# Kernel tuning notes

Measured on AMD Instinct MI355X. Metric: run time of the kernel, lower is better.

## Reference

```python
import jax, jax.numpy as jnp
import numpy as np

MIN_NORM = 1e-15
BALL_EPS = 4e-3  # torch float32 ball epsilon in KGEmb
E, R, D = 500000, 1000, 256
NQ = 200000
INIT = 1e-3
SCALE = float(1.0 / np.sqrt(D))


def setup_inputs() -> dict:
    key = jax.random.key(0)
    ks = jax.random.split(key, 7)
    heads = jax.random.randint(ks[0], (NQ, 1), 0, E)
    rels = jax.random.randint(ks[1], (NQ, 1), 0, R)
    tails = jax.random.randint(ks[2], (NQ, 1), 0, E)
    queries = jnp.concatenate([heads, rels, tails], axis=1)
    return {
        "queries": queries,
        "entity_emb": INIT * jax.random.normal(ks[3], (E, D), jnp.float32),
        "rel_emb": INIT * jax.random.normal(ks[4], (R, 2 * D), jnp.float32),
        "bias_head": jnp.zeros((E, 1), jnp.float32),
        "bias_tail": jnp.zeros((E, 1), jnp.float32),
        "c": jnp.ones((R, 1), jnp.float32),
        "att_rel_emb": 2.0 * jax.random.uniform(ks[5], (R, 2 * D), jnp.float32) - 1.0,
        "context_emb": INIT * jax.random.normal(ks[6], (R, D), jnp.float32),
    }


def artanh(x):
    x = jnp.clip(x, -1.0 + 1e-5, 1.0 - 1e-5)
    return 0.5 * (jnp.log1p(x) - jnp.log1p(-x))


def givens_rotations(r, x):
    # r, x: [n, d]; operate on d/2 independent 2-vectors
    n, d = x.shape
    g = r.reshape(n, d // 2, 2)
    g = g / jnp.maximum(jnp.linalg.norm(g, axis=-1, keepdims=True), MIN_NORM)
    xr = x.reshape(n, d // 2, 2)
    rot = jnp.stack(
        [g[..., 0] * xr[..., 0] - g[..., 1] * xr[..., 1],
         g[..., 0] * xr[..., 1] + g[..., 1] * xr[..., 0]], axis=-1)
    return rot.reshape(n, d)


def givens_reflection(r, x):
    n, d = x.shape
    g = r.reshape(n, d // 2, 2)
    g = g / jnp.maximum(jnp.linalg.norm(g, axis=-1, keepdims=True), MIN_NORM)
    xr = x.reshape(n, d // 2, 2)
    ref = jnp.stack(
        [g[..., 0] * xr[..., 0] + g[..., 1] * xr[..., 1],
         g[..., 1] * xr[..., 0] - g[..., 0] * xr[..., 1]], axis=-1)
    return ref.reshape(n, d)


def project(x, c):
    norm = jnp.maximum(jnp.linalg.norm(x, axis=-1, keepdims=True), MIN_NORM)
    maxnorm = (1.0 - BALL_EPS) / jnp.sqrt(c)
    return jnp.where(norm > maxnorm, x / norm * maxnorm, x)


def expmap0(u, c):
    sqrt_c = jnp.sqrt(c)
    u_norm = jnp.maximum(jnp.linalg.norm(u, axis=-1, keepdims=True), MIN_NORM)
    gamma_1 = jnp.tanh(sqrt_c * u_norm) * u / (sqrt_c * u_norm)
    return project(gamma_1, c)


def mobius_add(x, y, c):
    x2 = jnp.sum(x * x, axis=-1, keepdims=True)
    y2 = jnp.sum(y * y, axis=-1, keepdims=True)
    xy = jnp.sum(x * y, axis=-1, keepdims=True)
    num = (1.0 + 2.0 * c * xy + c * y2) * x + (1.0 - c * x2) * y
    denom = 1.0 + 2.0 * c * xy + (c ** 2) * x2 * y2
    return num / jnp.maximum(denom, MIN_NORM)


def hyp_distance(x, v, c):
    # x: point on ball, v: Euclidean (tangent) embedding; train mode (paired rows)
    sqrt_c = jnp.sqrt(c)
    vnorm = jnp.maximum(jnp.linalg.norm(v, axis=-1, keepdims=True), MIN_NORM)
    xv = jnp.sum(x * v / vnorm, axis=-1, keepdims=True)
    gamma = jnp.tanh(sqrt_c * vnorm) / vnorm
    x2 = jnp.sum(x * x, axis=-1, keepdims=True)
    c1 = 1.0 - 2.0 * c * gamma * xv + c * gamma ** 2
    c2 = 1.0 - c * x2
    num = jnp.sqrt(jnp.maximum((c1 ** 2) * x2 + (c2 ** 2) * (gamma ** 2)
                               - 2.0 * c1 * c2 * gamma * xv, 0.0))
    denom = jnp.maximum(1.0 - 2.0 * c * gamma * xv + (c ** 2) * (gamma ** 2) * x2, MIN_NORM)
    return 2.0 * artanh(sqrt_c * num / denom) / sqrt_c


def atth_forward(queries, entity_emb, rel_emb, bias_head, bias_tail, c,
                 att_rel_emb, context_emb):
    h, r, t = queries[:, 0], queries[:, 1], queries[:, 2]
    c_q = jax.nn.softplus(c[r])                       # [n, 1]
    head = entity_emb[h]                              # [n, D]
    rot_mat, ref_mat = jnp.split(att_rel_emb[r], 2, axis=1)
    rot_q = givens_rotations(rot_mat, head)           # [n, D]
    ref_q = givens_reflection(ref_mat, head)          # [n, D]
    cands = jnp.stack([ref_q, rot_q], axis=1)         # [n, 2, D]
    ctx = context_emb[r][:, None, :]                  # [n, 1, D]
    att_w = jax.nn.softmax(
        jnp.sum(ctx * cands * SCALE, axis=-1, keepdims=True), axis=1)  # [n, 2, 1]
    att_q = jnp.sum(att_w * cands, axis=1)            # [n, D]
    lhs = expmap0(att_q, c_q)
    rel = jnp.split(rel_emb[r], 2, axis=1)[0]
    rel = expmap0(rel, c_q)
    res = project(mobius_add(lhs, rel, c_q), c_q)
    dist2 = hyp_distance(res, entity_emb[t], c_q) ** 2
    predictions = bias_head[h] + bias_tail[t] + dist2  # [n, 1]
    factors = (head, rel_emb[r], entity_emb[t])
    return (predictions,) + factors


def reference(queries, entity_emb, rel_emb, bias_head, bias_tail, c,
              att_rel_emb, context_emb):
    return atth_forward(queries, entity_emb, rel_emb, bias_head, bias_tail, c,
                        att_rel_emb, context_emb)
```

## Files before the change

### kernel.cpp

```cpp
#include <hip/hip_runtime.h>
#include <math.h>

#define MIN_NORM 1e-15f
#define BALL_EPS 0.004f

constexpr int D  = 256;
constexpr int R  = 1000;
constexpr int NQ = 200000;
constexpr float SCALE = 0.0625f;

typedef float  f32x4  __attribute__((ext_vector_type(4)));
typedef unsigned short u16x8 __attribute__((ext_vector_type(8)));

__device__ __forceinline__ void nt_store4(float* p, f32x4 v) {
    __builtin_nontemporal_store(v, (f32x4*)p);
}
__device__ __forceinline__ f32x4 ld4(const float* p) { return *(const f32x4*)p; }

__device__ __forceinline__ unsigned short f2bf(float x) {
    unsigned int u = __float_as_uint(x);
    u += 0x7fffu + ((u >> 16) & 1u);
    return (unsigned short)(u >> 16);
}
__device__ __forceinline__ float bf2f(unsigned short u) {
    return __uint_as_float(((unsigned int)u) << 16);
}

__device__ __forceinline__ void half_sum4(float& a, float& b, float& c, float& d) {
    #pragma unroll
    for (int off = 16; off > 0; off >>= 1) {
        a += __shfl_xor(a, off, 64);
        b += __shfl_xor(b, off, 64);
        c += __shfl_xor(c, off, 64);
        d += __shfl_xor(d, off, 64);
    }
}
__device__ __forceinline__ void half_sum3(float& a, float& b, float& c) {
    #pragma unroll
    for (int off = 16; off > 0; off >>= 1) {
        a += __shfl_xor(a, off, 64);
        b += __shfl_xor(b, off, 64);
        c += __shfl_xor(c, off, 64);
    }
}

__device__ __forceinline__ void unpack8(f32x4 a, f32x4 b, float* d) {
    d[0] = a.x; d[1] = a.y; d[2] = a.z; d[3] = a.w;
    d[4] = b.x; d[5] = b.y; d[6] = b.z; d[7] = b.w;
}

__device__ __forceinline__ float tanh_pos(float x) {
    const float e = __expf(-2.0f * x);
    return (1.0f - e) / (1.0f + e);
}

__global__ __launch_bounds__(64) void prep_kernel(
    const float* __restrict__ rel_emb,
    const float* __restrict__ c_arr,
    const float* __restrict__ att_rel_emb,
    const float* __restrict__ context_emb,
    float* __restrict__ ws_scal,
    unsigned short* __restrict__ ws_rot,
    unsigned short* __restrict__ ws_ref,
    unsigned short* __restrict__ ws_ctx)
{
    const int r    = blockIdx.x;
    const int lane = threadIdx.x;

    const float craw   = c_arr[r];
    const float cq     = fmaxf(craw, 0.0f) + log1pf(__expf(-fabsf(craw)));
    const float sqrt_c = sqrtf(cq);
    const float maxnorm = (1.0f - BALL_EPS) / sqrt_c;

    const float* am = att_rel_emb + (size_t)r * 2 * D + lane * 4;
    const float* cb = context_emb + (size_t)r * D     + lane * 4;
    const float* rr = rel_emb     + (size_t)r * 2 * D + lane * 4;

    float rotn[4], refn[4];
    #pragma unroll
    for (int p = 0; p < 2; ++p) {
        const float a0 = am[2*p], a1 = am[2*p+1];
        float inv = rsqrtf(fmaxf(a0*a0 + a1*a1, 1e-30f));
        rotn[2*p] = a0*inv; rotn[2*p+1] = a1*inv;
        const float b0 = am[D + 2*p], b1 = am[D + 2*p+1];
        inv = rsqrtf(fmaxf(b0*b0 + b1*b1, 1e-30f));
        refn[2*p] = b0*inv; refn[2*p+1] = b1*inv;
    }

    float url2 = 0.0f;
    float ctxs[4];
    #pragma unroll
    for (int j = 0; j < 4; ++j) {
        ctxs[j] = cb[j] * SCALE;
        const float v = rr[j];
        url2 += v * v;
    }
    #pragma unroll
    for (int off = 32; off > 0; off >>= 1) url2 += __shfl_xor(url2, off, 64);

    const float url  = fmaxf(sqrtf(url2), MIN_NORM);
    const float facB = tanh_pos(sqrt_c * url) / (sqrt_c * url);
    const float nB   = facB * url;
    const float sB   = facB * ((nB > maxnorm) ? maxnorm / nB : 1.0f);
    const float y2   = sB * sB * url2;

    #pragma unroll
    for (int j = 0; j < 4; ++j) {
        ws_rot[(size_t)r * D + lane*4 + j] = f2bf(rotn[j]);
        ws_ref[(size_t)r * D + lane*4 + j] = f2bf(refn[j]);
        ws_ctx[(size_t)r * D + lane*4 + j] = f2bf(ctxs[j]);
    }
    if (lane == 0) {
        float* s = ws_scal + (size_t)r * 8;
        s[0] = cq; s[1] = sqrt_c; s[2] = maxnorm; s[3] = sB; s[4] = y2;
    }
}

__global__ __launch_bounds__(256) void atth_kernel(
    const int*   __restrict__ queries,
    const float* __restrict__ entity_emb,
    const float* __restrict__ rel_emb,
    const float* __restrict__ bias_head,
    const float* __restrict__ bias_tail,
    const float* __restrict__ ws_scal,
    const unsigned short* __restrict__ ws_rot,
    const unsigned short* __restrict__ ws_ref,
    const unsigned short* __restrict__ ws_ctx,
    float*       __restrict__ out)
{
    const int lane = threadIdx.x & 63;
    const int hl   = lane & 31;
    const int qid  = blockIdx.x * 8 + (threadIdx.x >> 5);
    if (qid >= NQ) return;

    const int h = queries[qid * 3 + 0];
    const int r = queries[qid * 3 + 1];
    const int t = queries[qid * 3 + 2];

    const float* sc = ws_scal + (size_t)r * 8;
    const float cq = sc[0], sqrt_c = sc[1], maxnorm = sc[2], sB = sc[3], y2 = sc[4];

    const int e8 = hl * 8;

    const float* eh = entity_emb + (size_t)h * D     + e8;
    const float* et = entity_emb + (size_t)t * D     + e8;
    const float* rr = rel_emb    + (size_t)r * 2 * D + e8;

    const f32x4 h0 = ld4(eh);     const f32x4 h1 = ld4(eh + 4);
    const f32x4 t0 = ld4(et);     const f32x4 t1 = ld4(et + 4);
    const f32x4 r0 = ld4(rr);     const f32x4 r1 = ld4(rr + 4);
    const f32x4 r2 = ld4(rr + D); const f32x4 r3 = ld4(rr + D + 4);
    const u16x8 rotv = *(const u16x8*)(ws_rot + (size_t)r * D + e8);
    const u16x8 refv = *(const u16x8*)(ws_ref + (size_t)r * D + e8);
    const u16x8 ctxv = *(const u16x8*)(ws_ctx + (size_t)r * D + e8);

    float* out_pred = out;
    float* out_head = out + (size_t)NQ;
    float* out_rel  = out + (size_t)NQ + (size_t)NQ * D;
    float* out_tail = out + (size_t)NQ + (size_t)NQ * D + (size_t)NQ * 2 * D;

    nt_store4(out_head + (size_t)qid * D         + e8,     h0);
    nt_store4(out_head + (size_t)qid * D         + e8 + 4, h1);
    nt_store4(out_rel  + (size_t)qid * 2 * D     + e8,     r0);
    nt_store4(out_rel  + (size_t)qid * 2 * D     + e8 + 4, r1);
    nt_store4(out_rel  + (size_t)qid * 2 * D + D + e8,     r2);
    nt_store4(out_rel  + (size_t)qid * 2 * D + D + e8 + 4, r3);
    nt_store4(out_tail + (size_t)qid * D         + e8,     t0);
    nt_store4(out_tail + (size_t)qid * D         + e8 + 4, t1);

    float hd[8], tl[8], rl[8];
    unpack8(h0, h1, hd);
    unpack8(t0, t1, tl);
    unpack8(r0, r1, rl);

    float rq[8], fq[8];
    #pragma unroll
    for (int p = 0; p < 4; ++p) {
        const int i0 = 2*p, i1 = 2*p + 1;
        const float g0 = bf2f(rotv[i0]), g1 = bf2f(rotv[i1]);
        rq[i0] = g0 * hd[i0] - g1 * hd[i1];
        rq[i1] = g0 * hd[i1] + g1 * hd[i0];
        const float e0 = bf2f(refv[i0]), e1 = bf2f(refv[i1]);
        fq[i0] = e0 * hd[i0] + e1 * hd[i1];
        fq[i1] = e1 * hd[i0] - e0 * hd[i1];
    }

    float sref = 0.0f, srot = 0.0f, sv = 0.0f, rtl = 0.0f;
    #pragma unroll
    for (int j = 0; j < 8; ++j) {
        const float cxj = bf2f(ctxv[j]);
        sref += cxj * fq[j];
        srot += cxj * rq[j];
        sv   += tl[j] * tl[j];
        rtl  += rl[j] * tl[j];
    }
    half_sum4(sref, srot, sv, rtl);

    const float mx   = fmaxf(sref, srot);
    const float eref = __expf(sref - mx), erot = __expf(srot - mx);
    const float inv_se = 1.0f / (eref + erot);
    const float wref = eref * inv_se, wrot = erot * inv_se;

    float att[8];
    #pragma unroll
    for (int j = 0; j < 8; ++j) att[j] = wref * fq[j] + wrot * rq[j];

    float u2 = 0.0f, adr = 0.0f, atl = 0.0f;
    #pragma unroll
    for (int j = 0; j < 8; ++j) {
        u2  += att[j] * att[j];
        adr += att[j] * rl[j];
        atl += att[j] * tl[j];
    }
    half_sum3(u2, adr, atl);

    const float u    = fmaxf(sqrtf(u2), MIN_NORM);
    const float facA = tanh_pos(sqrt_c * u) / (sqrt_c * u);
    const float nA   = facA * u;
    const float sA   = facA * ((nA > maxnorm) ? maxnorm / nA : 1.0f);
    const float x2   = sA * sA * u2;

    const float xy = sA * sB * adr;

    const float ka  = 1.0f + 2.0f * cq * xy + cq * y2;
    const float kb  = 1.0f - cq * x2;
    const float den = fmaxf(1.0f + 2.0f * cq * xy + cq * cq * x2 * y2, MIN_NORM);
    const float pA  = ka * sA / den;
    const float pB  = kb * sB / den;

    const float url2_from_y2 = 0.0f;
    (void)url2_from_y2;
    const float rl2 = y2 / fmaxf(sB * sB, 1e-30f);
    const float rn2 = pA*pA*u2 + 2.0f*pA*pB*adr + pB*pB*rl2;
    const float nrm = fmaxf(sqrtf(rn2), MIN_NORM);
    const float pr  = (nrm > maxnorm) ? maxnorm / nrm : 1.0f;
    const float rx2 = rn2 * pr * pr;

    const float vnorm = fmaxf(sqrtf(sv), MIN_NORM);
    const float sxv   = (pA * atl + pB * rtl) * pr;
    const float xv    = sxv / vnorm;
    const float gamma = tanh_pos(sqrt_c * vnorm) / vnorm;
    const float k1 = 1.0f - 2.0f * cq * gamma * xv + cq * gamma * gamma;
    const float k2 = 1.0f - cq * rx2;
    const float num = sqrtf(fmaxf(k1*k1*rx2 + k2*k2*gamma*gamma
                                  - 2.0f*k1*k2*gamma*xv, 0.0f));
    const float dden = fmaxf(1.0f - 2.0f*cq*gamma*xv + cq*cq*gamma*gamma*rx2, MIN_NORM);
    float arg = sqrt_c * num / dden;
    arg = fminf(fmaxf(arg, -1.0f + 1e-5f), 1.0f - 1e-5f);
    const float ath  = 0.5f * __logf((1.0f + arg) / (1.0f - arg));
    const float dist = 2.0f * ath / sqrt_c;
    const float dist2 = dist * dist;

    if (hl == 0) {
        __builtin_nontemporal_store(bias_head[h] + bias_tail[t] + dist2, out_pred + qid);
    }
}

extern "C" void kernel_launch(void* const* d_in, const int* in_sizes, int n_in,
                              void* d_out, int out_size, void* d_ws, size_t ws_size,
                              hipStream_t stream) {
    const int*   queries     = (const int*)  d_in[0];
    const float* entity_emb  = (const float*)d_in[1];
    const float* rel_emb     = (const float*)d_in[2];
    const float* bias_head   = (const float*)d_in[3];
    const float* bias_tail   = (const float*)d_in[4];
    const float* c_arr       = (const float*)d_in[5];
    const float* att_rel_emb = (const float*)d_in[6];
    const float* context_emb = (const float*)d_in[7];
    float* out = (float*)d_out;

    float*          ws_scal = (float*)d_ws;
    unsigned short* ws_rot  = (unsigned short*)(ws_scal + (size_t)R * 8);
    unsigned short* ws_ref  = ws_rot + (size_t)R * D;
    unsigned short* ws_ctx  = ws_ref + (size_t)R * D;

    prep_kernel<<<R, 64, 0, stream>>>(rel_emb, c_arr, att_rel_emb, context_emb,
                                      ws_scal, ws_rot, ws_ref, ws_ctx);

    const int queries_per_block = 8;
    const int grid = (NQ + queries_per_block - 1) / queries_per_block;
    atth_kernel<<<grid, 256, 0, stream>>>(queries, entity_emb, rel_emb,
                                          bias_head, bias_tail,
                                          ws_scal, ws_rot, ws_ref, ws_ctx, out);
}
```

Measured before the change: 304.8 us.

## Split rel_emb gather-copy into its own kernel and use bf16 rel in compute

Moves the copy of rel_emb rows into the output into a separate kernel where each wave copies one full 2D-float row. The main kernel instead reads a bf16 copy of the first half of the relation embedding prepared per relation, and a precomputed squared norm. This is meant to make the output write simpler and shrink the main kernel's per-query reads and stores. The cost is one extra kernel launch that re-reads the queries, and reduced precision for the relation vector in the distance math.

```diff
diff --git a/kernel.cpp b/kernel.cpp
--- a/kernel.cpp
+++ b/kernel.cpp
@@ -62,7 +62,8 @@
     float* __restrict__ ws_scal,
     unsigned short* __restrict__ ws_rot,
     unsigned short* __restrict__ ws_ref,
-    unsigned short* __restrict__ ws_ctx)
+    unsigned short* __restrict__ ws_ctx,
+    unsigned short* __restrict__ ws_rl)
 {
     const int r    = blockIdx.x;
     const int lane = threadIdx.x;
@@ -88,12 +89,12 @@
     }
 
     float url2 = 0.0f;
-    float ctxs[4];
+    float rlv[4], ctxs[4];
     #pragma unroll
     for (int j = 0; j < 4; ++j) {
         ctxs[j] = cb[j] * SCALE;
-        const float v = rr[j];
-        url2 += v * v;
+        rlv[j]  = rr[j];
+        url2 += rlv[j] * rlv[j];
     }
     #pragma unroll
     for (int off = 32; off > 0; off >>= 1) url2 += __shfl_xor(url2, off, 64);
@@ -109,23 +110,43 @@
         ws_rot[(size_t)r * D + lane*4 + j] = f2bf(rotn[j]);
         ws_ref[(size_t)r * D + lane*4 + j] = f2bf(refn[j]);
         ws_ctx[(size_t)r * D + lane*4 + j] = f2bf(ctxs[j]);
+        ws_rl [(size_t)r * D + lane*4 + j] = f2bf(rlv[j]);
     }
     if (lane == 0) {
         float* s = ws_scal + (size_t)r * 8;
         s[0] = cq; s[1] = sqrt_c; s[2] = maxnorm; s[3] = sB; s[4] = y2;
-    }
+        s[5] = url2;
+    }
+}
+
+__global__ __launch_bounds__(256) void copy_rel_kernel(
+    const int*   __restrict__ queries,
+    const float* __restrict__ rel_emb,
+    float*       __restrict__ out_rel)
+{
+    const int wave = threadIdx.x >> 6;
+    const int lane = threadIdx.x & 63;
+    const int q = blockIdx.x * 4 + wave;
+    if (q >= NQ) return;
+    const int r = queries[q * 3 + 1];
+    const float* src = rel_emb + (size_t)r * 2 * D + lane * 8;
+    float*       dst = out_rel + (size_t)q * 2 * D + lane * 8;
+    const f32x4 a = ld4(src);
+    const f32x4 b = ld4(src + 4);
+    nt_store4(dst,     a);
+    nt_store4(dst + 4, b);
 }
 
 __global__ __launch_bounds__(256) void atth_kernel(
     const int*   __restrict__ queries,
     const float* __restrict__ entity_emb,
-    const float* __restrict__ rel_emb,
     const float* __restrict__ bias_head,
     const float* __restrict__ bias_tail,
     const float* __restrict__ ws_scal,
     const unsigned short* __restrict__ ws_rot,
     const unsigned short* __restrict__ ws_ref,
     const unsigned short* __restrict__ ws_ctx,
+    const unsigned short* __restrict__ ws_rl,
     float*       __restrict__ out)
 {
     const int lane = threadIdx.x & 63;
@@ -139,39 +160,34 @@
 
     const float* sc = ws_scal + (size_t)r * 8;
     const float cq = sc[0], sqrt_c = sc[1], maxnorm = sc[2], sB = sc[3], y2 = sc[4];
+    const float rl2 = sc[5];
 
     const int e8 = hl * 8;
 
-    const float* eh = entity_emb + (size_t)h * D     + e8;
-    const float* et = entity_emb + (size_t)t * D     + e8;
-    const float* rr = rel_emb    + (size_t)r * 2 * D + e8;
+    const float* eh = entity_emb + (size_t)h * D + e8;
+    const float* et = entity_emb + (size_t)t * D + e8;
 
     const f32x4 h0 = ld4(eh);     const f32x4 h1 = ld4(eh + 4);
     const f32x4 t0 = ld4(et);     const f32x4 t1 = ld4(et + 4);
-    const f32x4 r0 = ld4(rr);     const f32x4 r1 = ld4(rr + 4);
-    const f32x4 r2 = ld4(rr + D); const f32x4 r3 = ld4(rr + D + 4);
     const u16x8 rotv = *(const u16x8*)(ws_rot + (size_t)r * D + e8);
     const u16x8 refv = *(const u16x8*)(ws_ref + (size_t)r * D + e8);
     const u16x8 ctxv = *(const u16x8*)(ws_ctx + (size_t)r * D + e8);
+    const u16x8 rlv  = *(const u16x8*)(ws_rl  + (size_t)r * D + e8);
 
     float* out_pred = out;
     float* out_head = out + (size_t)NQ;
-    float* out_rel  = out + (size_t)NQ + (size_t)NQ * D;
     float* out_tail = out + (size_t)NQ + (size_t)NQ * D + (size_t)NQ * 2 * D;
 
-    nt_store4(out_head + (size_t)qid * D         + e8,     h0);
-    nt_store4(out_head + (size_t)qid * D         + e8 + 4, h1);
-    nt_store4(out_rel  + (size_t)qid * 2 * D     + e8,     r0);
-    nt_store4(out_rel  + (size_t)qid * 2 * D     + e8 + 4, r1);
-    nt_store4(out_rel  + (size_t)qid * 2 * D + D + e8,     r2);
-    nt_store4(out_rel  + (size_t)qid * 2 * D + D + e8 + 4, r3);
-    nt_store4(out_tail + (size_t)qid * D         + e8,     t0);
-    nt_store4(out_tail + (size_t)qid * D         + e8 + 4, t1);
+    nt_store4(out_head + (size_t)qid * D + e8,     h0);
+    nt_store4(out_head + (size_t)qid * D + e8 + 4, h1);
+    nt_store4(out_tail + (size_t)qid * D + e8,     t0);
+    nt_store4(out_tail + (size_t)qid * D + e8 + 4, t1);
 
     float hd[8], tl[8], rl[8];
     unpack8(h0, h1, hd);
     unpack8(t0, t1, tl);
-    unpack8(r0, r1, rl);
+    #pragma unroll
+    for (int j = 0; j < 8; ++j) rl[j] = bf2f(rlv[j]);
 
     float rq[8], fq[8];
     #pragma unroll
@@ -228,9 +244,6 @@
     const float pA  = ka * sA / den;
     const float pB  = kb * sB / den;
 
-    const float url2_from_y2 = 0.0f;
-    (void)url2_from_y2;
-    const float rl2 = y2 / fmaxf(sB * sB, 1e-30f);
     const float rn2 = pA*pA*u2 + 2.0f*pA*pB*adr + pB*pB*rl2;
     const float nrm = fmaxf(sqrtf(rn2), MIN_NORM);
     const float pr  = (nrm > maxnorm) ? maxnorm / nrm : 1.0f;
@@ -273,13 +286,19 @@
     unsigned short* ws_rot  = (unsigned short*)(ws_scal + (size_t)R * 8);
     unsigned short* ws_ref  = ws_rot + (size_t)R * D;
     unsigned short* ws_ctx  = ws_ref + (size_t)R * D;
+    unsigned short* ws_rl   = ws_ctx + (size_t)R * D;
+
+    float* out_rel = out + (size_t)NQ + (size_t)NQ * D;
 
     prep_kernel<<<R, 64, 0, stream>>>(rel_emb, c_arr, att_rel_emb, context_emb,
-                                      ws_scal, ws_rot, ws_ref, ws_ctx);
+                                      ws_scal, ws_rot, ws_ref, ws_ctx, ws_rl);
+
+    copy_rel_kernel<<<(NQ + 3) / 4, 256, 0, stream>>>(queries, rel_emb, out_rel);
 
     const int queries_per_block = 8;
     const int grid = (NQ + queries_per_block - 1) / queries_per_block;
-    atth_kernel<<<grid, 256, 0, stream>>>(queries, entity_emb, rel_emb,
+    atth_kernel<<<grid, 256, 0, stream>>>(queries, entity_emb,
                                           bias_head, bias_tail,
-                                          ws_scal, ws_rot, ws_ref, ws_ctx, out);
-}
+                                          ws_scal, ws_rot, ws_ref, ws_ctx, ws_rl,
+                                          out);
+}
```

Result: slower. 359.2 us (+17.8%).
